# Kernel optimization log

Measured on AMD Instinct MI355X. Metric: run time of the kernel, lower is better.

## Reference

```python
import jax, jax.numpy as jnp
import numpy as np

NUM_EXPERTS = 8
TOP_K = 2
D = 512
F = 2048
B, L = 4, 1024


def setup_inputs() -> dict:
    key = jax.random.key(0)
    ks = jax.random.split(key, 5)
    std = D ** -0.5
    return {
        "x": jax.random.normal(ks[0], (B, L, D), jnp.float32),
        "gate_w": jax.random.normal(ks[1], (NUM_EXPERTS, D), jnp.float32) * std,
        "w1": jax.random.normal(ks[2], (NUM_EXPERTS, F, D), jnp.float32) * std,
        "w2": jax.random.normal(ks[3], (NUM_EXPERTS, D, F), jnp.float32) * (F ** -0.5),
        "w3": jax.random.normal(ks[4], (NUM_EXPERTS, F, D), jnp.float32) * std,
    }


def reference(x, gate_w, w1, w2, w3):
    b, l, d = x.shape
    xf = x.reshape(-1, d)                      # [T, D]
    T = xf.shape[0]
    router_logits = xf @ gate_w.T              # [T, E]
    # top-k routing in float32 (as in original), softmax over selected logits
    topk_w, topk_idx = jax.lax.top_k(router_logits.astype(jnp.float32), TOP_K)
    topk_w = jax.nn.softmax(topk_w, axis=-1).astype(x.dtype)  # [T, K]
    # combine weights per (token, expert): scatter top-k weights into dense [T, E]
    cw = jnp.zeros((T, NUM_EXPERTS), x.dtype)
    cw = cw.at[jnp.arange(T)[:, None], topk_idx].add(topk_w)
    # per-expert gated FFN (SiLU(x w1^T) * (x w3^T)) w2^T, batched over experts
    h = jax.nn.silu(jnp.einsum('td,efd->etf', xf, w1)) * jnp.einsum('td,efd->etf', xf, w3)
    y = jnp.einsum('etf,edf->etd', h, w2)      # [E, T, D]
    out = jnp.einsum('te,etd->td', cw, y)      # weighted combine
    return out.reshape(b, l, d), router_logits
```

## Files before the change

kernel.cpp:

```cpp
#include <hip/hip_runtime.h>

#define TTOK 4096
#define NEXP 8
#define DDIM 512
#define FDIM 2048
#define HROWS 8576

typedef __attribute__((ext_vector_type(8))) short short8;
typedef __attribute__((ext_vector_type(4))) float floatx4;

#define BAR()  __builtin_amdgcn_s_barrier()
#define SBAR() __builtin_amdgcn_sched_barrier(0)

__device__ __forceinline__ ushort f2b(float f) {
  unsigned u = __float_as_uint(f);
  u += 0x7fffu + ((u >> 16) & 1u);
  return (ushort)(u >> 16);
}

__device__ __forceinline__ void load16(void* lds, const void* g) {
  __builtin_amdgcn_global_load_lds(
      (const __attribute__((address_space(1))) unsigned int*)g,
      (__attribute__((address_space(3))) unsigned int*)lds, 16, 0, 0);
}


__global__ __launch_bounds__(256) void k_front(
    const float* __restrict__ x, const float* __restrict__ gw,
    float* __restrict__ logits, int* __restrict__ tok_e,
    float2* __restrict__ tok_w, float* __restrict__ outz,
    const float* __restrict__ w1, ushort* __restrict__ w1t,
    const float* __restrict__ w3, ushort* __restrict__ w3t)
{
  __shared__ ushort sm[4096];
  const int tid = threadIdx.x;
  if (blockIdx.x < TTOK / 4) {
    float4 zz = {0.f, 0.f, 0.f, 0.f};
    float4* orow = (float4*)(outz + (size_t)blockIdx.x * 4 * DDIM);
    orow[tid] = zz;
    orow[tid + 256] = zz;
    const int lane = tid & 63;
    const int t = blockIdx.x * 4 + (tid >> 6);
    float xv[8];
#pragma unroll
    for (int i = 0; i < 8; ++i) xv[i] = x[(size_t)t * DDIM + lane + 64 * i];
    float lg[8];
#pragma unroll
    for (int e = 0; e < 8; ++e) {
      float a = 0.f;
#pragma unroll
      for (int i = 0; i < 8; ++i) a += xv[i] * gw[e * DDIM + lane + 64 * i];
#pragma unroll
      for (int s = 32; s; s >>= 1) a += __shfl_xor(a, s, 64);
      lg[e] = a;
    }
    if (lane < 8) logits[(size_t)t * 8 + lane] = lg[lane];
    if (lane == 0) {
      int i0 = 0; float v0 = lg[0];
#pragma unroll
      for (int e = 1; e < 8; ++e) { if (lg[e] > v0) { v0 = lg[e]; i0 = e; } }
      int i1 = -1; float v1 = -3.4e38f;
#pragma unroll
      for (int e = 0; e < 8; ++e) { if (e != i0 && lg[e] > v1) { v1 = lg[e]; i1 = e; } }
      float ex = expf(v1 - v0);
      float inv = 1.f / (1.f + ex);
      tok_e[t] = i0 | (i1 << 4);
      tok_w[t] = make_float2(inv, ex * inv);
    }
    return;
  }
  int bid = blockIdx.x - TTOK / 4;
  const float* src = (bid < 2048) ? w1 : w3;
  ushort* dst = (bid < 2048) ? w1t : w3t;
  if (bid >= 2048) bid -= 2048;
  const int r0 = (bid >> 2) * 32;
  const int c0 = (bid & 3) * 128;
#pragma unroll
  for (int i = 0; i < 4; ++i) {
    int j = i * 1024 + tid * 4;
    int lr = j >> 7, lc = j & 127;
    float4 v = *(const float4*)&src[(size_t)(r0 + lr) * 512 + c0 + lc];
    ushort4 b = { f2b(v.x), f2b(v.y), f2b(v.z), f2b(v.w) };
    int ord = (lr >> 4) * 4 + (lc >> 5);
    int slot = (lr & 15) + 16 * ((lc >> 3) & 3);
    *(ushort4*)&sm[(ord * 64 + slot) * 8 + (lc & 7)] = b;
  }
  __syncthreads();
  const size_t tb0 = ((size_t)(r0 >> 4) * 16 + (c0 >> 5)) * 512;
#pragma unroll
  for (int rt = 0; rt < 2; ++rt)
    *(short8*)&dst[tb0 + (size_t)rt * 16 * 512 + tid * 8] =
        *(const short8*)&sm[rt * 2048 + tid * 8];
}

__global__ __launch_bounds__(1024) void k_build(
    const int* __restrict__ tok_e, const float2* __restrict__ tok_w,
    int* __restrict__ counts, int* __restrict__ lists, float* __restrict__ wts)
{
  const int e = blockIdx.x;
  const int tid = threadIdx.x;
  const int lane = tid & 63, wid = tid >> 6;
  __shared__ int wcnt[16];
  __shared__ int sbase;
  if (tid == 0) sbase = 0;
  __syncthreads();

  for (int c = 0; c < TTOK; c += 1024) {
    int t = c + tid;
    int pe = tok_e[t];
    bool m0 = (pe & 15) == e;
    bool m1 = ((pe >> 4) & 15) == e;
    bool m = m0 || m1;
    unsigned long long b = __ballot(m);
    int lpre = __popcll(b & ((1ull << lane) - 1ull));
    if (lane == 0) wcnt[wid] = __popcll(b);
    __syncthreads();
    int woff = 0;
#pragma unroll
    for (int i = 0; i < 16; ++i) if (i < wid) woff += wcnt[i];
    if (m) {
      float2 w = tok_w[t];
      int pos = sbase + woff + lpre;
      lists[e * TTOK + pos] = t;
      wts[e * TTOK + pos] = m0 ? w.x : w.y;
    }
    __syncthreads();
    if (tid == 0) {
      int s = 0;
#pragma unroll
      for (int i = 0; i < 16; ++i) s += wcnt[i];
      sbase += s;
    }
    __syncthreads();
  }
  if (tid == 0) counts[e] = sbase;
}

__global__ __launch_bounds__(256) void k_gather(
    const float* __restrict__ x, const int* __restrict__ counts,
    const int* __restrict__ lists, ushort* __restrict__ Xg)
{
  int pp[9];
  pp[0] = 0;
#pragma unroll
  for (int i = 0; i < 8; ++i) pp[i + 1] = pp[i] + ((counts[i] + 31) & ~31);
  int gid = blockIdx.x * 256 + threadIdx.x;
  int gr = gid >> 6, dg = gid & 63;
  if (gr >= pp[8]) return;
  int e = 0;
  while (e < 7 && gr >= pp[e + 1]) ++e;
  int p = gr - pp[e];
  size_t dst = ((size_t)(gr >> 4) * 16 + (dg >> 2)) * 512
             + ((gr & 15) + 16 * (dg & 3)) * 8;
  short8 o = (short8)0;
  if (p < counts[e]) {
    int t = lists[e * TTOK + p];
    const float* s = x + (size_t)t * DDIM + dg * 8;
    float4 a = *(const float4*)s;
    float4 b = *(const float4*)(s + 4);
    o[0] = f2b(a.x); o[1] = f2b(a.y); o[2] = f2b(a.z); o[3] = f2b(a.w);
    o[4] = f2b(b.x); o[5] = f2b(b.y); o[6] = f2b(b.z); o[7] = f2b(b.w);
  }
  *(short8*)&Xg[dst] = o;
}

__global__ __launch_bounds__(512) void k_ffn1(
    const ushort* __restrict__ Xg, const ushort* __restrict__ w1t,
    const ushort* __restrict__ w3t, const int* __restrict__ counts,
    ushort* __restrict__ H,
    const float* __restrict__ w2, ushort* __restrict__ w2t)
{
  __shared__ ushort Xls[2][4096], W1ls[2][4096], W3ls[2][4096];
  const int tid = threadIdx.x;

  const int grp = blockIdx.x >> 3, lane8 = blockIdx.x & 7;
  const int q3 = grp % 3, gq = grp / 3;

  if (q3 == 2) {
    int bid = gq * 8 + lane8;
    ushort* sm = &Xls[0][0];
    const int r0 = (bid >> 4) * 32;
    const int c0 = (bid & 15) * 128;
#pragma unroll
    for (int i = 0; i < 2; ++i) {
      int j = i * 2048 + tid * 4;
      int lr = j >> 7, lc = j & 127;
      float4 v = *(const float4*)&w2[(size_t)(r0 + lr) * 2048 + c0 + lc];
      ushort4 b = { f2b(v.x), f2b(v.y), f2b(v.z), f2b(v.w) };
      int ord = (lr >> 4) * 4 + (lc >> 5);
      int slot = (lr & 15) + 16 * ((lc >> 3) & 3);
      *(ushort4*)&sm[(ord * 64 + slot) * 8 + (lc & 7)] = b;
    }
    __syncthreads();
    const size_t tb0 = ((size_t)(r0 >> 4) * 64 + (c0 >> 5)) * 512;
    int rt = tid >> 8, s = tid & 255;
    *(short8*)&w2t[tb0 + (size_t)rt * 64 * 512 + s * 8] =
        *(const short8*)&sm[rt * 2048 + s * 8];
    return;
  }

  const int gemmid = (gq * 2 + q3) * 8 + lane8;
  const int widx = (gemmid & 7) * 512 + (gemmid >> 3);
  const int mt = widx & 31, e = (widx >> 5) & 7, ft = widx >> 8;
  const int ne = counts[e];
  const int m0 = mt * 128;
  if (m0 >= ne) return;
  const int f0 = ft * 128;
  int hb = 0;
#pragma unroll
  for (int i = 0; i < 7; ++i) if (i < e) hb += (counts[i] + 31) & ~31;
  const int wid = tid >> 6, lane = tid & 63;
  const int wm = wid >> 2, wn = wid & 3;
  const int lr = lane & 15, lgp = lane >> 4;

  const int rtX0 = (hb + m0) >> 4;
  const ushort* sx = Xg  + ((size_t)(rtX0 + wid) * 16) * 512 + lane * 8;
  const ushort* s1 = w1t + ((size_t)(e * 128 + (f0 >> 4) + wid) * 16) * 512 + lane * 8;
  const ushort* s3 = w3t + ((size_t)(e * 128 + (f0 >> 4) + wid) * 16) * 512 + lane * 8;

#define FFN1_STAGE(B)                                                       \
  { load16((char*)&Xls[B][0]  + wid * 1024, sx);                            \
    load16((char*)&W1ls[B][0] + wid * 1024, s1);                            \
    load16((char*)&W3ls[B][0] + wid * 1024, s3);                            \
    sx += 512; s1 += 512; s3 += 512; }

#define FFN1_COMPUTE(B)                                                     \
  { short8 af[4], b1[2], b3[2];                                             \
    _Pragma("unroll")                                                       \
    for (int mf = 0; mf < 4; ++mf)                                          \
      af[mf] = *(const short8*)&Xls[B][(wm * 4 + mf) * 512 + lane * 8];     \
    _Pragma("unroll")                                                       \
    for (int nf = 0; nf < 2; ++nf) {                                        \
      b1[nf] = *(const short8*)&W1ls[B][(wn * 2 + nf) * 512 + lane * 8];    \
      b3[nf] = *(const short8*)&W3ls[B][(wn * 2 + nf) * 512 + lane * 8];    \
    }                                                                       \
    _Pragma("unroll")                                                       \
    for (int mf = 0; mf < 4; ++mf)                                          \
      _Pragma("unroll")                                                     \
      for (int nf = 0; nf < 2; ++nf) {                                      \
        acc1[mf][nf] = __builtin_amdgcn_mfma_f32_16x16x32_bf16(             \
            af[mf], b1[nf], acc1[mf][nf], 0, 0, 0);                         \
        acc3[mf][nf] = __builtin_amdgcn_mfma_f32_16x16x32_bf16(             \
            af[mf], b3[nf], acc3[mf][nf], 0, 0, 0);                         \
      } }

  floatx4 acc1[4][2], acc3[4][2];
#pragma unroll
  for (int a = 0; a < 4; ++a)
#pragma unroll
    for (int b = 0; b < 2; ++b) { acc1[a][b] = (floatx4)0.f; acc3[a][b] = (floatx4)0.f; }

  FFN1_STAGE(0);
  for (int t = 0; t < 16; t += 2) {
    FFN1_STAGE(1);
    asm volatile("s_waitcnt vmcnt(3)" ::: "memory");
    BAR(); SBAR();
    FFN1_COMPUTE(0);
    SBAR(); BAR();
    if (t + 2 < 16) {
      FFN1_STAGE(0);
      asm volatile("s_waitcnt vmcnt(3)" ::: "memory");
    } else {
      asm volatile("s_waitcnt vmcnt(0)" ::: "memory");
    }
    BAR(); SBAR();
    FFN1_COMPUTE(1);
    SBAR(); BAR();
  }

#pragma unroll
  for (int mf = 0; mf < 4; ++mf) {
    const int rtOut = rtX0 + wm * 4 + mf;
#pragma unroll
    for (int nf = 0; nf < 2; ++nf) {
      const int kt = (f0 >> 5) + wn;
      const int slotc = (nf * 2 + (lr >> 3)) & 3;
      size_t base = ((size_t)rtOut * 64 + kt) * 512 + 16 * slotc * 8 + (lr & 7);
      floatx4 v1 = acc1[mf][nf], v3 = acc3[mf][nf];
#pragma unroll
      for (int j = 0; j < 4; ++j) {
        int p = m0 + wm * 64 + mf * 16 + lgp * 4 + j;
        if (p < ne) {
          float h1 = v1[j], h3 = v3[j];
          float sig = 1.f / (1.f + __expf(-h1));
          H[base + (size_t)(lgp * 4 + j) * 8] = f2b(h1 * sig * h3);
        }
      }
    }
  }
#undef FFN1_STAGE
#undef FFN1_COMPUTE
}

__global__ __launch_bounds__(512) void k_ffn2(
    const ushort* __restrict__ Ht, const ushort* __restrict__ w2t,
    const int* __restrict__ counts, const int* __restrict__ lists,
    const float* __restrict__ wts, float* __restrict__ out)
{
  const int bid = blockIdx.x;
  const int widx = (bid & 7) * 256 + (bid >> 3);
  const int mt = widx & 31, e = (widx >> 5) & 7;
  const int rest = widx >> 8;
  const int dt = rest & 3, ks = rest >> 2;
  const int ne = counts[e];
  const int m0 = mt * 128;
  if (m0 >= ne) return;
  const int d0 = dt * 128;
  int hb = 0;
#pragma unroll
  for (int i = 0; i < 7; ++i) if (i < e) hb += (counts[i] + 31) & ~31;
  const int tid = threadIdx.x;
  const int wid = tid >> 6, lane = tid & 63;
  const int wm = wid >> 2, wn = wid & 3;
  const int lr = lane & 15, lgp = lane >> 4;

  __shared__ ushort Hls[2][8192], W2ls[2][8192];
  __shared__ int toks[128];
  __shared__ float twt[128];

  if (tid < 128) {
    int p = m0 + tid;
    bool v = p < ne;
    toks[tid] = v ? lists[e * TTOK + p] : 0;
    twt[tid] = v ? wts[e * TTOK + p] : 0.f;
  }

  const int rtH0 = (hb + m0) >> 4;
  const int kb = ks * 32;
  const ushort* sh = Ht  + ((size_t)(rtH0 + wid) * 64 + kb) * 512 + lane * 8;
  const ushort* sw = w2t + ((size_t)(e * 32 + (d0 >> 4) + wid) * 64 + kb) * 512 + lane * 8;

#define FFN2_STAGE(B)                                                      \
  { load16((char*)&Hls[B][0]  + (wid * 2) * 1024, sh);                     \
    load16((char*)&Hls[B][0]  + (wid * 2 + 1) * 1024, sh + 512);           \
    load16((char*)&W2ls[B][0] + (wid * 2) * 1024, sw);                     \
    load16((char*)&W2ls[B][0] + (wid * 2 + 1) * 1024, sw + 512);           \
    sh += 1024; sw += 1024; }

#define FFN2_COMPUTE(B)                                                    \
  { _Pragma("unroll")                                                      \
    for (int kk = 0; kk < 2; ++kk) {                                       \
      short8 af[4], bf[2];                                                 \
      _Pragma("unroll")                                                    \
      for (int mf = 0; mf < 4; ++mf)                                       \
        af[mf] = *(const short8*)&Hls[B][((wm * 4 + mf) * 2 + kk) * 512 + lane * 8]; \
      _Pragma("unroll")                                                    \
      for (int nf = 0; nf < 2; ++nf)                                       \
        bf[nf] = *(const short8*)&W2ls[B][((wn * 2 + nf) * 2 + kk) * 512 + lane * 8]; \
      _Pragma("unroll")                                                    \
      for (int mf = 0; mf < 4; ++mf)                                       \
        _Pragma("unroll")                                                  \
        for (int nf = 0; nf < 2; ++nf)                                     \
          acc[mf][nf] = __builtin_amdgcn_mfma_f32_16x16x32_bf16(           \
              af[mf], bf[nf], acc[mf][nf], 0, 0, 0);                       \
    } }

  floatx4 acc[4][2];
#pragma unroll
  for (int a = 0; a < 4; ++a)
#pragma unroll
    for (int b = 0; b < 2; ++b) acc[a][b] = (floatx4)0.f;

  FFN2_STAGE(0);
  for (int t = 0; t < 16; t += 2) {
    FFN2_STAGE(1);
    asm volatile("s_waitcnt vmcnt(4)" ::: "memory");
    BAR(); SBAR();
    FFN2_COMPUTE(0);
    SBAR(); BAR();
    if (t + 2 < 16) {
      FFN2_STAGE(0);
      asm volatile("s_waitcnt vmcnt(4)" ::: "memory");
    } else {
      asm volatile("s_waitcnt vmcnt(0)" ::: "memory");
    }
    BAR(); SBAR();
    FFN2_COMPUTE(1);
    SBAR(); BAR();
  }

#pragma unroll
  for (int mf = 0; mf < 4; ++mf) {
#pragma unroll
    for (int j = 0; j < 4; ++j) {
      int rloc = wm * 64 + mf * 16 + lgp * 4 + j;
      int p = m0 + rloc;
      if (p < ne) {
        int t = toks[rloc];
        float w = twt[rloc];
#pragma unroll
        for (int nf = 0; nf < 2; ++nf) {
          int d = d0 + wn * 32 + nf * 16 + lr;
          atomicAdd(&out[(size_t)t * DDIM + d], w * acc[mf][nf][j]);
        }
      }
    }
  }
#undef FFN2_STAGE
#undef FFN2_COMPUTE
}

extern "C" void kernel_launch(void* const* d_in, const int* in_sizes, int n_in,
                              void* d_out, int out_size, void* d_ws, size_t ws_size,
                              hipStream_t stream) {
  const float* x  = (const float*)d_in[0];
  const float* gw = (const float*)d_in[1];
  const float* w1 = (const float*)d_in[2];
  const float* w2 = (const float*)d_in[3];
  const float* w3 = (const float*)d_in[4];
  float* out = (float*)d_out;
  float* logits = out + (size_t)TTOK * DDIM;

  int* counts = (int*)d_ws;
  int* tok_e  = counts + 16;
  float2* tok_w = (float2*)(tok_e + TTOK);
  int* lists  = (int*)(tok_w + TTOK);
  float* wts  = (float*)(lists + NEXP * TTOK);
  ushort* w1t = (ushort*)(wts + NEXP * TTOK);
  ushort* w3t = w1t + (size_t)NEXP * FDIM * DDIM;
  ushort* w2t = w3t + (size_t)NEXP * FDIM * DDIM;
  ushort* Xg  = w2t + (size_t)NEXP * DDIM * FDIM;
  ushort* H   = Xg + (size_t)HROWS * DDIM;

  k_front<<<TTOK / 4 + 4096, 256, 0, stream>>>(x, gw, logits, tok_e, tok_w,
                                               out, w1, w1t, w3, w3t);
  k_build<<<NEXP, 1024, 0, stream>>>(tok_e, tok_w, counts, lists, wts);
  k_gather<<<(8448 * 64) / 256, 256, 0, stream>>>(x, counts, lists, Xg);

  k_ffn1<<<4096 + 2048, 512, 0, stream>>>(Xg, w1t, w3t, counts, H, w2, w2t);
  k_ffn2<<<2048, 512, 0, stream>>>(H, w2t, counts, lists, wts, out);
}
```

Before: 143.3 us.

## Triple-buffer FFN1 LDS staging to keep two global loads in flight

Replaces the double-buffered LDS staging in the FFN1 GEMM with a three-stage ring buffer in a single shared array and fully unrolls the K loop. Each iteration issues the load two tiles ahead and waits only until the current tile has arrived, so more global-to-LDS latency is hidden behind MFMA work. LDS use per block grows from 48KB to 72KB, which may lower occupancy, and the larger unrolled loop raises code size.

```diff
diff --git a/kernel.cpp b/kernel.cpp
--- a/kernel.cpp
+++ b/kernel.cpp
@@ -170,7 +170,7 @@
     ushort* __restrict__ H,
     const float* __restrict__ w2, ushort* __restrict__ w2t)
 {
-  __shared__ ushort Xls[2][4096], W1ls[2][4096], W3ls[2][4096];
+  __shared__ ushort smem[36864];
   const int tid = threadIdx.x;
 
   const int grp = blockIdx.x >> 3, lane8 = blockIdx.x & 7;
@@ -178,7 +178,7 @@
 
   if (q3 == 2) {
     int bid = gq * 8 + lane8;
-    ushort* sm = &Xls[0][0];
+    ushort* sm = smem;
     const int r0 = (bid >> 4) * 32;
     const int c0 = (bid & 15) * 128;
 #pragma unroll
@@ -219,20 +219,22 @@
   const ushort* s3 = w3t + ((size_t)(e * 128 + (f0 >> 4) + wid) * 16) * 512 + lane * 8;
 
 #define FFN1_STAGE(B)                                                       \
-  { load16((char*)&Xls[B][0]  + wid * 1024, sx);                            \
-    load16((char*)&W1ls[B][0] + wid * 1024, s1);                            \
-    load16((char*)&W3ls[B][0] + wid * 1024, s3);                            \
+  { char* base = (char*)smem + (B) * 24576 + wid * 1024;                    \
+    load16(base, sx);                                                       \
+    load16(base + 8192, s1);                                                \
+    load16(base + 16384, s3);                                               \
     sx += 512; s1 += 512; s3 += 512; }
 
 #define FFN1_COMPUTE(B)                                                     \
-  { short8 af[4], b1[2], b3[2];                                             \
+  { const ushort* cb = smem + (B) * 12288;                                  \
+    short8 af[4], b1[2], b3[2];                                             \
     _Pragma("unroll")                                                       \
     for (int mf = 0; mf < 4; ++mf)                                          \
-      af[mf] = *(const short8*)&Xls[B][(wm * 4 + mf) * 512 + lane * 8];     \
+      af[mf] = *(const short8*)&cb[(wm * 4 + mf) * 512 + lane * 8];         \
     _Pragma("unroll")                                                       \
     for (int nf = 0; nf < 2; ++nf) {                                        \
-      b1[nf] = *(const short8*)&W1ls[B][(wn * 2 + nf) * 512 + lane * 8];    \
-      b3[nf] = *(const short8*)&W3ls[B][(wn * 2 + nf) * 512 + lane * 8];    \
+      b1[nf] = *(const short8*)&cb[4096 + (wn * 2 + nf) * 512 + lane * 8];  \
+      b3[nf] = *(const short8*)&cb[8192 + (wn * 2 + nf) * 512 + lane * 8];  \
     }                                                                       \
     _Pragma("unroll")                                                       \
     for (int mf = 0; mf < 4; ++mf)                                          \
@@ -251,20 +253,15 @@
     for (int b = 0; b < 2; ++b) { acc1[a][b] = (floatx4)0.f; acc3[a][b] = (floatx4)0.f; }
 
   FFN1_STAGE(0);
-  for (int t = 0; t < 16; t += 2) {
-    FFN1_STAGE(1);
-    asm volatile("s_waitcnt vmcnt(3)" ::: "memory");
+  FFN1_STAGE(1);
+#pragma unroll
+  for (int t = 0; t < 16; ++t) {
+    if (t + 2 < 16) FFN1_STAGE((t + 2) % 3);
+    if (t < 14)      asm volatile("s_waitcnt vmcnt(6)" ::: "memory");
+    else if (t < 15) asm volatile("s_waitcnt vmcnt(3)" ::: "memory");
+    else             asm volatile("s_waitcnt vmcnt(0)" ::: "memory");
     BAR(); SBAR();
-    FFN1_COMPUTE(0);
-    SBAR(); BAR();
-    if (t + 2 < 16) {
-      FFN1_STAGE(0);
-      asm volatile("s_waitcnt vmcnt(3)" ::: "memory");
-    } else {
-      asm volatile("s_waitcnt vmcnt(0)" ::: "memory");
-    }
-    BAR(); SBAR();
-    FFN1_COMPUTE(1);
+    FFN1_COMPUTE(t % 3);
     SBAR(); BAR();
   }
 
```

New measurement: 138.6 us. -3.3%, faster.
